# Performance work log

Hardware: AMD Instinct MI355X
Metric: run time of the kernel (lower is better)

The kernel has to match this reference:

```python
import jax, jax.numpy as jnp
import numpy as np

DIM = 384
WIN = 7
HEADS = 12
N = WIN * WIN  # 49
NUM_WINDOWS = 64
B_W = 2048


def _relative_position_index():
    coords = np.stack(np.meshgrid(np.arange(WIN), np.arange(WIN), indexing='ij'))  # (2,W,W)
    cf = coords.reshape(2, -1)  # (2,N)
    rel = cf[:, :, None] - cf[:, None, :]  # (2,N,N)
    rel = rel.transpose(1, 2, 0)
    rel[:, :, 0] += WIN - 1
    rel[:, :, 1] += WIN - 1
    rel[:, :, 0] *= 2 * WIN - 1
    return jnp.asarray(rel.sum(-1), dtype=jnp.int32)  # (N,N)


def setup_inputs() -> dict:
    key = jax.random.key(0)
    ks = jax.random.split(key, 8)
    x = jax.random.normal(ks[0], (B_W, N, DIM), dtype=jnp.float32)
    m = jax.random.uniform(ks[1], (NUM_WINDOWS, N, N))
    mask = jnp.where(m < 0.1, -100.0, 0.0).astype(jnp.float32)
    sd = 0.02
    qkv_w = jax.random.normal(ks[2], (DIM, 3 * DIM), dtype=jnp.float32) * sd
    qkv_b = jnp.zeros((3 * DIM,), dtype=jnp.float32)
    proj_w = jax.random.normal(ks[3], (DIM, DIM), dtype=jnp.float32) * sd
    proj_b = jnp.zeros((DIM,), dtype=jnp.float32)
    bias_table = jax.random.normal(ks[4], ((2 * WIN - 1) ** 2, HEADS), dtype=jnp.float32) * sd
    rel_idx = _relative_position_index()
    return {"x": x, "mask": mask, "qkv_w": qkv_w, "qkv_b": qkv_b,
            "proj_w": proj_w, "proj_b": proj_b, "bias_table": bias_table,
            "rel_idx": rel_idx}


def reference(x, mask, qkv_w, qkv_b, proj_w, proj_b, bias_table, rel_idx):
    Bw, n, C = x.shape
    H = HEADS
    hd = C // H
    scale = hd ** -0.5
    qkv = (x @ qkv_w + qkv_b).reshape(Bw, n, 3, H, hd)
    qkv = jnp.transpose(qkv, (2, 0, 3, 1, 4))  # (3, Bw, H, N, hd)
    q, k, v = qkv[0], qkv[1], qkv[2]
    attn = jnp.einsum('bhnd,bhmd->bhnm', q * scale, k)  # (Bw,H,N,N)
    bias = bias_table[rel_idx.reshape(-1)].reshape(n, n, H)
    attn = attn + jnp.transpose(bias, (2, 0, 1))[None]
    nW = mask.shape[0]
    attn = attn.reshape(Bw // nW, nW, H, n, n) + mask[None, :, None]
    attn = attn.reshape(Bw, H, n, n)
    attn = jax.nn.softmax(attn, axis=-1)
    out = jnp.einsum('bhnm,bhmd->bhnd', attn, v)
    out = jnp.transpose(out, (0, 2, 1, 3)).reshape(Bw, n, C)
    return out @ proj_w + proj_b
```

## Files before the change

### kernel.cpp

```cpp
#include <hip/hip_runtime.h>


#define DIMC   384
#define NTOK   49
#define NHEAD  12
#define HD     32
#define NWIN   64
#define BWIN   2048
#define SCALE  0.17677669529663687f

#define SLOT     4704
#define NBQ      9
#define NBP      3
#define FRAG_BLK 8192

#define WS_SLOTS ((size_t)BWIN * NHEAD * SLOT)
#define WS_BFRAG ((size_t)NBQ * 12 * FRAG_BLK)
#define WS_PFRAG ((size_t)NBP * 12 * FRAG_BLK)
#define WS_COMB  ((size_t)NWIN * NHEAD * NTOK * 64)
#define WS_NEED  ((WS_SLOTS + WS_BFRAG + WS_PFRAG) * 2 + WS_COMB * 4)

typedef short bf16x8 __attribute__((ext_vector_type(8)));
typedef unsigned short u16x8 __attribute__((ext_vector_type(8)));
typedef unsigned u32x4 __attribute__((ext_vector_type(4)));
typedef float f32x4  __attribute__((ext_vector_type(4)));

__device__ __forceinline__ unsigned short f2bf(float f) {
    union { float f; unsigned u; } v; v.f = f;
    unsigned r = v.u + 0x7fffu + ((v.u >> 16) & 1u);
    return (unsigned short)(r >> 16);
}
__device__ __forceinline__ float bf2f(unsigned short h) {
    union { unsigned u; float f; } v; v.u = ((unsigned)h) << 16;
    return v.f;
}
__device__ __forceinline__ void split2(float x, unsigned short& hi, unsigned short& lo) {
    hi = f2bf(x);
    lo = f2bf(x - bf2f(hi));
}
__device__ __forceinline__ unsigned cvtpk(float a, float b) {
    unsigned r;
    asm("v_cvt_pk_bf16_f32 %0, %1, %2" : "=v"(r) : "v"(a), "v"(b));
    return r;
}
__device__ __forceinline__ unsigned lopk(float a, float b, unsigned h) {
    union { unsigned u; float f; } h0, h1;
    h0.u = h << 16; h1.u = h & 0xffff0000u;
    return cvtpk(a - h0.f, b - h1.f);
}
__device__ __forceinline__ void splitpk8(float4 a, float4 b, u32x4& h, u32x4& l) {
    h[0] = cvtpk(a.x, a.y); h[1] = cvtpk(a.z, a.w);
    h[2] = cvtpk(b.x, b.y); h[3] = cvtpk(b.z, b.w);
    l[0] = lopk(a.x, a.y, h[0]); l[1] = lopk(a.z, a.w, h[1]);
    l[2] = lopk(b.x, b.y, h[2]); l[3] = lopk(b.z, b.w, h[3]);
}
__device__ __forceinline__ float4 ld4(const float* p) {
    return *reinterpret_cast<const float4*>(p);
}
__device__ __forceinline__ void gload16(const unsigned short* g, unsigned short* l) {
    __builtin_amdgcn_global_load_lds(
        (const __attribute__((address_space(1))) void*)g,
        (__attribute__((address_space(3))) void*)l, 16, 0, 0);
}

__global__ __launch_bounds__(256) void k_prep_w(
    const float* __restrict__ w, unsigned short* __restrict__ dst, int ncols)
{
    int f = blockIdx.x * 256 + threadIdx.x;
    if (f >= ncols * 48) return;
    int nb = f / 6144, rem = f - nb * 6144;
    int kc = rem >> 9, rem2 = rem & 511;
    int kq = rem2 >> 7, rl = rem2 & 127;
    int n = nb * 128 + rl, k0 = kc * 32 + kq * 8;
    u16x8 h8, l8;
    #pragma unroll
    for (int e = 0; e < 8; ++e) {
        unsigned short hh, ll;
        split2(w[(size_t)(k0 + e) * ncols + n], hh, ll);
        h8[e] = hh; l8[e] = ll;
    }
    size_t base = ((size_t)(nb * 12 + kc) << 13) + (size_t)((kq << 7) + rl) * 8;
    *reinterpret_cast<u16x8*>(&dst[base])        = h8;
    *reinterpret_cast<u16x8*>(&dst[base + 4096]) = l8;
}

__global__ __launch_bounds__(256) void k_prep_comb(
    const float* __restrict__ mask, const float* __restrict__ bias_table,
    const int* __restrict__ rel_idx, float* __restrict__ comb)
{
    int wh = blockIdx.x;
    int w = wh / NHEAD, h = wh - w * NHEAD;
    float* dst = comb + (size_t)wh * (NTOK * 64);
    for (int o = threadIdx.x; o < NTOK * 64; o += 256) {
        int i = o >> 6, j = o & 63;
        float v = -1e9f;
        if (j < NTOK) {
            int o2 = i * NTOK + j;
            v = mask[w * NTOK * NTOK + o2] + bias_table[rel_idx[o2] * NHEAD + h];
        }
        dst[o] = v;
    }
}

__global__ __launch_bounds__(256) void k_gemm_qkv(
    const float* __restrict__ x, const unsigned short* __restrict__ Bfrag,
    const float* __restrict__ qb, unsigned short* __restrict__ ws)
{
    __shared__ __align__(16) unsigned short Als[FRAG_BLK];
    __shared__ __align__(16) unsigned short Bls[FRAG_BLK];

    const int t = threadIdx.x;
    const int wave = t >> 6, l = t & 63, lj = l & 15, quad = l >> 4;
    const int wm = wave & 1, wn = wave >> 1;
    const int gm0 = blockIdx.y * 128, gn0 = blockIdx.x * 128;

    const int fs0 = t, fs1 = t + 256;
    const float* xp0 = x + (size_t)(gm0 + (fs0 & 127)) * DIMC + (fs0 >> 7) * 8;
    const float* xp1 = x + (size_t)(gm0 + (fs1 & 127)) * DIMC + (fs1 >> 7) * 8;
    const unsigned short* Bg = Bfrag + (size_t)blockIdx.x * 12 * FRAG_BLK;

    f32x4 acc[4][4];
    #pragma unroll
    for (int i = 0; i < 4; ++i)
        #pragma unroll
        for (int j = 0; j < 4; ++j) acc[i][j] = (f32x4)0.0f;

    for (int kc = 0; kc < 12; ++kc) {
        #pragma unroll
        for (int c = 0; c < 4; ++c) {
            int ch = wave * 4 + c;
            gload16(Bg + (size_t)kc * FRAG_BLK + ch * 512 + l * 8, &Bls[ch * 512]);
        }
        {
            float4 x0 = ld4(xp0 + kc * 32), x1 = ld4(xp0 + kc * 32 + 4);
            u32x4 h, lo;
            splitpk8(x0, x1, h, lo);
            *reinterpret_cast<u32x4*>(&Als[fs0 * 8])        = h;
            *reinterpret_cast<u32x4*>(&Als[4096 + fs0 * 8]) = lo;
        }
        {
            float4 x0 = ld4(xp1 + kc * 32), x1 = ld4(xp1 + kc * 32 + 4);
            u32x4 h, lo;
            splitpk8(x0, x1, h, lo);
            *reinterpret_cast<u32x4*>(&Als[fs1 * 8])        = h;
            *reinterpret_cast<u32x4*>(&Als[4096 + fs1 * 8]) = lo;
        }
        __syncthreads();

        bf16x8 ah[4], al[4], bh[4], bl[4];
        #pragma unroll
        for (int i = 0; i < 4; ++i) {
            int ra = (quad * 128 + wm * 64 + i * 16 + lj) * 8;
            ah[i] = *reinterpret_cast<const bf16x8*>(&Als[ra]);
            al[i] = *reinterpret_cast<const bf16x8*>(&Als[4096 + ra]);
            int rb = (quad * 128 + wn * 64 + i * 16 + lj) * 8;
            bh[i] = *reinterpret_cast<const bf16x8*>(&Bls[rb]);
            bl[i] = *reinterpret_cast<const bf16x8*>(&Bls[4096 + rb]);
        }
        #pragma unroll
        for (int tm = 0; tm < 4; ++tm)
            #pragma unroll
            for (int tn = 0; tn < 4; ++tn) {
                acc[tm][tn] = __builtin_amdgcn_mfma_f32_16x16x32_bf16(ah[tm], bh[tn], acc[tm][tn], 0, 0, 0);
                acc[tm][tn] = __builtin_amdgcn_mfma_f32_16x16x32_bf16(ah[tm], bl[tn], acc[tm][tn], 0, 0, 0);
                acc[tm][tn] = __builtin_amdgcn_mfma_f32_16x16x32_bf16(al[tm], bh[tn], acc[tm][tn], 0, 0, 0);
            }
        __syncthreads();
    }

    #pragma unroll
    for (int tn = 0; tn < 4; ++tn) {
        int col = gn0 + wn * 64 + tn * 16 + lj;
        float bias = qb[col];
        int part = col / 384, rem = col - part * 384;
        int h = rem >> 5, d = rem & 31;
        #pragma unroll
        for (int tm = 0; tm < 4; ++tm) {
            #pragma unroll
            for (int rr = 0; rr < 4; ++rr) {
                int row = gm0 + wm * 64 + tm * 16 + quad * 4 + rr;
                int b = row / 49, n = row - b * 49;
                size_t off = ((size_t)(b * NHEAD + h) * 3 + part) * 1568 + n * HD + d;
                ws[off] = f2bf(acc[tm][tn][rr] + bias);
            }
        }
    }
}

__global__ __launch_bounds__(128) void k_attn_mfma(
    unsigned short* __restrict__ ws, const float* __restrict__ comb)
{
    __shared__ __align__(16) unsigned short Pimg[2][8192];
    __shared__ __align__(16) unsigned short Vts[2][2048];

    const int t = threadIdx.x, wave = t >> 6, l = t & 63;
    const int lj = l & 15, quad = l >> 4;
    const int idx = blockIdx.x * 2 + wave;
    const int b = idx / NHEAD, h = idx - b * NHEAD;
    unsigned short* qp = ws + (size_t)idx * SLOT;
    const float* cb = comb + (size_t)((b & (NWIN - 1)) * NHEAD + h) * (NTOK * 64);
    unsigned short* pimg = Pimg[wave];
    unsigned short* vt   = Vts[wave];

    #pragma unroll
    for (int it = 0; it < 4; ++it)
        *reinterpret_cast<u16x8*>(&vt[it * 512 + l * 8]) = (u16x8)0;

    u16x8 vc[4];
    #pragma unroll
    for (int it = 0; it < 4; ++it) {
        int c = it * 64 + l;
        vc[it] = (c < 196)
            ? *reinterpret_cast<const u16x8*>(qp + 3136 + (c >> 2) * HD + (c & 3) * 8)
            : (u16x8)0;
    }

    bf16x8 aq[4], bk[4];
    #pragma unroll
    for (int mt = 0; mt < 4; ++mt) {
        int row = mt * 16 + lj;
        aq[mt] = (row < NTOK)
            ? *reinterpret_cast<const bf16x8*>(qp + row * HD + quad * 8) : (bf16x8)0;
        bk[mt] = (row < NTOK)
            ? *reinterpret_cast<const bf16x8*>(qp + 1568 + row * HD + quad * 8) : (bf16x8)0;
    }

    f32x4 s[4][4];
    #pragma unroll
    for (int mt = 0; mt < 4; ++mt)
        #pragma unroll
        for (int nt = 0; nt < 4; ++nt)
            s[mt][nt] = __builtin_amdgcn_mfma_f32_16x16x32_bf16(aq[mt], bk[nt], (f32x4)0.0f, 0, 0, 0);

    #pragma unroll
    for (int mt = 0; mt < 4; ++mt)
        #pragma unroll
        for (int r = 0; r < 4; ++r) {
            int i = mt * 16 + quad * 4 + r;
            #pragma unroll
            for (int nt = 0; nt < 4; ++nt) {
                float c = (i < NTOK) ? cb[i * 64 + nt * 16 + lj] : -1e9f;
                s[mt][nt][r] = fmaf(s[mt][nt][r], SCALE, c);
            }
        }

    __syncthreads();

    #pragma unroll
    for (int it = 0; it < 4; ++it) {
        int c = it * 64 + l;
        if (c < 196) {
            int j = c >> 2, dq = c & 3;
            #pragma unroll
            for (int e = 0; e < 8; ++e) {
                int d = dq * 8 + e;
                vt[(d * 64 + j) ^ ((d & 7) << 3)] = (unsigned short)vc[it][e];
            }
        }
    }

    #pragma unroll
    for (int mt = 0; mt < 4; ++mt)
        #pragma unroll
        for (int r = 0; r < 4; ++r) {
            float m = fmaxf(fmaxf(s[mt][0][r], s[mt][1][r]),
                            fmaxf(s[mt][2][r], s[mt][3][r]));
            m = fmaxf(m, __shfl_xor(m, 1));
            m = fmaxf(m, __shfl_xor(m, 2));
            m = fmaxf(m, __shfl_xor(m, 4));
            m = fmaxf(m, __shfl_xor(m, 8));
            float e0 = __expf(s[mt][0][r] - m), e1 = __expf(s[mt][1][r] - m);
            float e2 = __expf(s[mt][2][r] - m), e3 = __expf(s[mt][3][r] - m);
            float sum = (e0 + e1) + (e2 + e3);
            sum += __shfl_xor(sum, 1);
            sum += __shfl_xor(sum, 2);
            sum += __shfl_xor(sum, 4);
            sum += __shfl_xor(sum, 8);
            float inv = 1.0f / sum;
            int i = mt * 16 + quad * 4 + r;
            int swz = (i & 7) << 3;
            float p0 = e0 * inv, p1 = e1 * inv, p2 = e2 * inv, p3 = e3 * inv;
            unsigned short hh, ll;
            split2(p0, hh, ll);
            pimg[(i * 64 +  0 + lj) ^ swz] = hh; pimg[4096 + ((i * 64 +  0 + lj) ^ swz)] = ll;
            split2(p1, hh, ll);
            pimg[(i * 64 + 16 + lj) ^ swz] = hh; pimg[4096 + ((i * 64 + 16 + lj) ^ swz)] = ll;
            split2(p2, hh, ll);
            pimg[(i * 64 + 32 + lj) ^ swz] = hh; pimg[4096 + ((i * 64 + 32 + lj) ^ swz)] = ll;
            split2(p3, hh, ll);
            pimg[(i * 64 + 48 + lj) ^ swz] = hh; pimg[4096 + ((i * 64 + 48 + lj) ^ swz)] = ll;
        }

    __syncthreads();

    f32x4 o[4][2];
    #pragma unroll
    for (int mt = 0; mt < 4; ++mt) { o[mt][0] = (f32x4)0.0f; o[mt][1] = (f32x4)0.0f; }
    #pragma unroll
    for (int ks = 0; ks < 2; ++ks) {
        bf16x8 bv[2];
        #pragma unroll
        for (int nt = 0; nt < 2; ++nt) {
            int d = nt * 16 + lj;
            bv[nt] = *reinterpret_cast<const bf16x8*>(
                &vt[(d * 64 + ks * 32 + quad * 8) ^ ((d & 7) << 3)]);
        }
        #pragma unroll
        for (int mt = 0; mt < 4; ++mt) {
            int i = mt * 16 + lj;
            int fo = (i * 64 + ks * 32 + quad * 8) ^ ((i & 7) << 3);
            bf16x8 ph = *reinterpret_cast<const bf16x8*>(&pimg[fo]);
            bf16x8 pl = *reinterpret_cast<const bf16x8*>(&pimg[4096 + fo]);
            #pragma unroll
            for (int nt = 0; nt < 2; ++nt) {
                o[mt][nt] = __builtin_amdgcn_mfma_f32_16x16x32_bf16(ph, bv[nt], o[mt][nt], 0, 0, 0);
                o[mt][nt] = __builtin_amdgcn_mfma_f32_16x16x32_bf16(pl, bv[nt], o[mt][nt], 0, 0, 0);
            }
        }
    }

    #pragma unroll
    for (int mt = 0; mt < 4; ++mt)
        #pragma unroll
        for (int r = 0; r < 4; ++r) {
            int i = mt * 16 + quad * 4 + r;
            if (i < NTOK) {
                qp[i * HD + lj]      = f2bf(o[mt][0][r]);
                qp[i * HD + 16 + lj] = f2bf(o[mt][1][r]);
            }
        }
}

__global__ __launch_bounds__(256) void k_gemm_proj(
    const unsigned short* __restrict__ ws, const unsigned short* __restrict__ Pfrag,
    const float* __restrict__ pbias, float* __restrict__ out)
{
    __shared__ __align__(16) unsigned short Als[4096];
    __shared__ __align__(16) unsigned short Bls[FRAG_BLK];

    const int t = threadIdx.x;
    const int wave = t >> 6, l = t & 63, lj = l & 15, quad = l >> 4;
    const int wm = wave & 1, wn = wave >> 1;
    const int gm0 = blockIdx.y * 128, gn0 = blockIdx.x * 128;

    const int ch0 = wave * 2, ch1 = wave * 2 + 1;
    size_t abase0, abase1;
    {
        int fs = ch0 * 64 + l;
        int kq = fs >> 7, rl = fs & 127, row = gm0 + rl;
        int b = row / 49, n = row - b * 49;
        abase0 = (size_t)(b * NHEAD) * SLOT + n * HD + kq * 8;
    }
    {
        int fs = ch1 * 64 + l;
        int kq = fs >> 7, rl = fs & 127, row = gm0 + rl;
        int b = row / 49, n = row - b * 49;
        abase1 = (size_t)(b * NHEAD) * SLOT + n * HD + kq * 8;
    }
    const unsigned short* Bg = Pfrag + (size_t)blockIdx.x * 12 * FRAG_BLK;

    f32x4 acc[4][4];
    #pragma unroll
    for (int i = 0; i < 4; ++i)
        #pragma unroll
        for (int j = 0; j < 4; ++j) acc[i][j] = (f32x4)0.0f;

    for (int kc = 0; kc < 12; ++kc) {
        #pragma unroll
        for (int c = 0; c < 4; ++c) {
            int ch = wave * 4 + c;
            gload16(Bg + (size_t)kc * FRAG_BLK + ch * 512 + l * 8, &Bls[ch * 512]);
        }
        gload16(ws + abase0 + (size_t)kc * SLOT, &Als[ch0 * 512]);
        gload16(ws + abase1 + (size_t)kc * SLOT, &Als[ch1 * 512]);
        __syncthreads();

        bf16x8 a[4], bh[4], bl[4];
        #pragma unroll
        for (int i = 0; i < 4; ++i) {
            a[i] = *reinterpret_cast<const bf16x8*>(&Als[(quad * 128 + wm * 64 + i * 16 + lj) * 8]);
            int rb = (quad * 128 + wn * 64 + i * 16 + lj) * 8;
            bh[i] = *reinterpret_cast<const bf16x8*>(&Bls[rb]);
            bl[i] = *reinterpret_cast<const bf16x8*>(&Bls[4096 + rb]);
        }
        #pragma unroll
        for (int tm = 0; tm < 4; ++tm)
            #pragma unroll
            for (int tn = 0; tn < 4; ++tn) {
                acc[tm][tn] = __builtin_amdgcn_mfma_f32_16x16x32_bf16(a[tm], bh[tn], acc[tm][tn], 0, 0, 0);
                acc[tm][tn] = __builtin_amdgcn_mfma_f32_16x16x32_bf16(a[tm], bl[tn], acc[tm][tn], 0, 0, 0);
            }
        __syncthreads();
    }

    #pragma unroll
    for (int tn = 0; tn < 4; ++tn) {
        int col = gn0 + wn * 64 + tn * 16 + lj;
        float bias = pbias[col];
        #pragma unroll
        for (int tm = 0; tm < 4; ++tm)
            #pragma unroll
            for (int rr = 0; rr < 4; ++rr) {
                int row = gm0 + wm * 64 + tm * 16 + quad * 4 + rr;
                out[(size_t)row * DIMC + col] = acc[tm][tn][rr] + bias;
            }
    }
}

__global__ __launch_bounds__(192) void k_qkv_attn(
    const float* __restrict__ x, const float* __restrict__ mask,
    const float* __restrict__ qkv_w, const float* __restrict__ qkv_b,
    const float* __restrict__ bias_table, const int* __restrict__ rel_idx,
    float* __restrict__ out)
{
    __shared__ __align__(16) float xs_t[64 * 68];
    __shared__ __align__(16) float qs[NTOK * HD];
    __shared__ __align__(16) float ks_[NTOK * HD];
    __shared__ __align__(16) float vs[NTOK * HD];
    __shared__ __align__(16) union { float w[64 * 96]; float s[NTOK * 56]; } u;

    const int t = threadIdx.x, b = blockIdx.x;
    const int tx = t % 12, ty = t / 12;
    const float* xb = x + (size_t)b * NTOK * DIMC;
    const int mbase = (b % NWIN) * NTOK * NTOK;

    for (int h = 0; h < NHEAD; ++h) {
        float acc[4][8];
        #pragma unroll
        for (int r = 0; r < 4; ++r)
            #pragma unroll
            for (int cc = 0; cc < 8; ++cc) acc[r][cc] = 0.0f;
        for (int c0 = 0; c0 < DIMC; c0 += 64) {
            for (int idx = t; idx < NTOK * 64; idx += 192) {
                int i = idx >> 6, kk2 = idx & 63;
                xs_t[kk2 * 68 + i] = xb[i * DIMC + c0 + kk2];
            }
            for (int idx = t; idx < 64 * 96; idx += 192) {
                int kk2 = idx / 96, c = idx % 96;
                int col = (c >> 5) * DIMC + h * HD + (c & 31);
                u.w[kk2 * 96 + c] = qkv_w[(size_t)(c0 + kk2) * (3 * DIMC) + col];
            }
            __syncthreads();
            #pragma unroll 8
            for (int kk2 = 0; kk2 < 64; ++kk2) {
                const float4 xv = ld4(&xs_t[kk2 * 68 + ty * 4]);
                const float4 w0 = ld4(&u.w[kk2 * 96 + tx * 8]);
                const float4 w1 = ld4(&u.w[kk2 * 96 + tx * 8 + 4]);
                const float xr[4] = {xv.x, xv.y, xv.z, xv.w};
                const float wc[8] = {w0.x, w0.y, w0.z, w0.w, w1.x, w1.y, w1.z, w1.w};
                #pragma unroll
                for (int r = 0; r < 4; ++r)
                    #pragma unroll
                    for (int cc = 0; cc < 8; ++cc)
                        acc[r][cc] = fmaf(xr[r], wc[cc], acc[r][cc]);
            }
            __syncthreads();
        }
        {
            const int part = tx >> 2, cbase = (tx & 3) * 8;
            float* dst = (part == 0) ? qs : (part == 1) ? ks_ : vs;
            #pragma unroll
            for (int r = 0; r < 4; ++r) {
                int i = ty * 4 + r;
                if (i < NTOK)
                    #pragma unroll
                    for (int cc = 0; cc < 8; ++cc) {
                        int c5 = cbase + cc;
                        dst[i * HD + c5] = acc[r][cc] + qkv_b[part * DIMC + h * HD + c5];
                    }
            }
        }
        __syncthreads();
        for (int o = t; o < NTOK * NTOK; o += 192) {
            int i = o / 49, j = o % 49;
            float4 a4 = {0.f, 0.f, 0.f, 0.f};
            #pragma unroll
            for (int seg = 0; seg < 8; ++seg) {
                float4 q4 = ld4(&qs[i * HD + seg * 4]);
                float4 k4 = ld4(&ks_[j * HD + seg * 4]);
                a4.x = fmaf(q4.x, k4.x, a4.x); a4.y = fmaf(q4.y, k4.y, a4.y);
                a4.z = fmaf(q4.z, k4.z, a4.z); a4.w = fmaf(q4.w, k4.w, a4.w);
            }
            u.s[i * 56 + j] = (a4.x + a4.y + a4.z + a4.w) * SCALE
                            + bias_table[rel_idx[o] * NHEAD + h] + mask[mbase + o];
        }
        __syncthreads();
        if (t < NTOK) {
            float* row = &u.s[t * 56];
            float m = row[0];
            for (int j = 1; j < NTOK; ++j) m = fmaxf(m, row[j]);
            float ssum = 0.f;
            for (int j = 0; j < NTOK; ++j) { float e = __expf(row[j] - m); row[j] = e; ssum += e; }
            float inv = 1.0f / ssum;
            for (int j = 0; j < NTOK; ++j) row[j] *= inv;
        }
        __syncthreads();
        for (int o = t; o < NTOK * 8; o += 192) {
            int i = o >> 3, dg = o & 7;
            float4 a = {0.f, 0.f, 0.f, 0.f};
            for (int j = 0; j < NTOK; ++j) {
                float sj = u.s[i * 56 + j];
                float4 v4 = ld4(&vs[j * HD + dg * 4]);
                a.x = fmaf(sj, v4.x, a.x); a.y = fmaf(sj, v4.y, a.y);
                a.z = fmaf(sj, v4.z, a.z); a.w = fmaf(sj, v4.w, a.w);
            }
            *reinterpret_cast<float4*>(&out[(size_t)(b * NTOK + i) * DIMC + h * HD + dg * 4]) = a;
        }
        __syncthreads();
    }
}

__global__ __launch_bounds__(192) void k_proj(
    float* __restrict__ io, const float* __restrict__ proj_w,
    const float* __restrict__ proj_b)
{
    __shared__ __align__(16) float ys_t[DIMC * 20];
    __shared__ __align__(16) float wch[16 * DIMC];
    const int t = threadIdx.x, row0 = blockIdx.x * 16;
    const int tx = t % 48, ty = t / 48;
    for (int idx = t; idx < 16 * DIMC; idx += 192) {
        int i = idx / DIMC, k = idx % DIMC;
        ys_t[k * 20 + i] = io[(size_t)(row0 + i) * DIMC + k];
    }
    float acc[4][8];
    #pragma unroll
    for (int r = 0; r < 4; ++r)
        #pragma unroll
        for (int cc = 0; cc < 8; ++cc) acc[r][cc] = 0.0f;
    for (int k0 = 0; k0 < DIMC; k0 += 16) {
        for (int idx = t; idx < 16 * DIMC; idx += 192) {
            int kk2 = idx / DIMC, c = idx % DIMC;
            wch[kk2 * DIMC + c] = proj_w[(size_t)(k0 + kk2) * DIMC + c];
        }
        __syncthreads();
        #pragma unroll
        for (int kk2 = 0; kk2 < 16; ++kk2) {
            const float4 xv = ld4(&ys_t[(k0 + kk2) * 20 + ty * 4]);
            const float4 w0 = ld4(&wch[kk2 * DIMC + tx * 8]);
            const float4 w1 = ld4(&wch[kk2 * DIMC + tx * 8 + 4]);
            const float xr[4] = {xv.x, xv.y, xv.z, xv.w};
            const float wc[8] = {w0.x, w0.y, w0.z, w0.w, w1.x, w1.y, w1.z, w1.w};
            #pragma unroll
            for (int r = 0; r < 4; ++r)
                #pragma unroll
                for (int cc = 0; cc < 8; ++cc)
                    acc[r][cc] = fmaf(xr[r], wc[cc], acc[r][cc]);
        }
        __syncthreads();
    }
    #pragma unroll
    for (int r = 0; r < 4; ++r) {
        int i = ty * 4 + r;
        float* dst = &io[(size_t)(row0 + i) * DIMC + tx * 8];
        #pragma unroll
        for (int cc = 0; cc < 8; ++cc) dst[cc] = acc[r][cc] + proj_b[tx * 8 + cc];
    }
}

extern "C" void kernel_launch(void* const* d_in, const int* in_sizes, int n_in,
                              void* d_out, int out_size, void* d_ws, size_t ws_size,
                              hipStream_t stream) {
    const float* x          = (const float*)d_in[0];
    const float* mask       = (const float*)d_in[1];
    const float* qkv_w      = (const float*)d_in[2];
    const float* qkv_b      = (const float*)d_in[3];
    const float* proj_w     = (const float*)d_in[4];
    const float* proj_b     = (const float*)d_in[5];
    const float* bias_table = (const float*)d_in[6];
    const int*   rel_idx    = (const int*)d_in[7];
    float* out = (float*)d_out;

    if (ws_size >= WS_NEED) {
        unsigned short* ws = (unsigned short*)d_ws;
        unsigned short* Bf = ws + WS_SLOTS;
        unsigned short* Pf = Bf + WS_BFRAG;
        float* combf = (float*)(Pf + WS_PFRAG);
        k_prep_w<<<216, 256, 0, stream>>>(qkv_w, Bf, 3 * DIMC);
        k_prep_w<<<72, 256, 0, stream>>>(proj_w, Pf, DIMC);
        k_prep_comb<<<NWIN * NHEAD, 256, 0, stream>>>(mask, bias_table, rel_idx, combf);
        dim3 g1(9, 784);
        k_gemm_qkv<<<g1, 256, 0, stream>>>(x, Bf, qkv_b, ws);
        k_attn_mfma<<<(BWIN * NHEAD) / 2, 128, 0, stream>>>(ws, combf);
        dim3 g3(3, 784);
        k_gemm_proj<<<g3, 256, 0, stream>>>(ws, Pf, proj_b, out);
    } else {
        k_qkv_attn<<<BWIN, 192, 0, stream>>>(x, mask, qkv_w, qkv_b,
                                             bias_table, rel_idx, out);
        k_proj<<<(BWIN * NTOK) / 16, 192, 0, stream>>>(out, proj_w, proj_b);
    }
}
```

Before: 815.5 us.

## Pre-split x into bf16 hi/lo fragment layout and swizzle GEMM block order

```diff
diff --git a/kernel.cpp b/kernel.cpp
--- a/kernel.cpp
+++ b/kernel.cpp
@@ -12,13 +12,16 @@
 #define SLOT     4704
 #define NBQ      9
 #define NBP      3
+#define NRP      784
 #define FRAG_BLK 8192
 
 #define WS_SLOTS ((size_t)BWIN * NHEAD * SLOT)
 #define WS_BFRAG ((size_t)NBQ * 12 * FRAG_BLK)
 #define WS_PFRAG ((size_t)NBP * 12 * FRAG_BLK)
+#define WS_XFRAG ((size_t)NRP * 12 * FRAG_BLK)
 #define WS_COMB  ((size_t)NWIN * NHEAD * NTOK * 64)
-#define WS_NEED  ((WS_SLOTS + WS_BFRAG + WS_PFRAG) * 2 + WS_COMB * 4)
+#define WS_NEED_MID  ((WS_SLOTS + WS_BFRAG + WS_PFRAG) * 2 + WS_COMB * 4)
+#define WS_NEED_FULL (WS_NEED_MID + WS_XFRAG * 2)
 
 typedef short bf16x8 __attribute__((ext_vector_type(8)));
 typedef unsigned short u16x8 __attribute__((ext_vector_type(8)));
@@ -82,6 +85,36 @@
     size_t base = ((size_t)(nb * 12 + kc) << 13) + (size_t)((kq << 7) + rl) * 8;
     *reinterpret_cast<u16x8*>(&dst[base])        = h8;
     *reinterpret_cast<u16x8*>(&dst[base + 4096]) = l8;
+}
+
+__global__ __launch_bounds__(256) void k_prep_x(
+    const float* __restrict__ x, unsigned short* __restrict__ xf)
+{
+    __shared__ __align__(16) unsigned short H[4096], L[4096];
+    const int bid = blockIdx.x, rp = bid / 12, kc = bid - rp * 12;
+    const int t = threadIdx.x;
+    const int row0 = t >> 3, c4 = t & 7;
+    #pragma unroll
+    for (int p = 0; p < 4; ++p) {
+        int row = p * 32 + row0;
+        float4 v = ld4(x + (size_t)(rp * 128 + row) * DIMC + kc * 32 + c4 * 4);
+        unsigned h0 = cvtpk(v.x, v.y), h1 = cvtpk(v.z, v.w);
+        unsigned l0 = lopk(v.x, v.y, h0), l1 = lopk(v.z, v.w, h1);
+        int off = ((c4 >> 1) * 128 + row) * 8 + (c4 & 1) * 4;
+        *reinterpret_cast<unsigned*>(&H[off])     = h0;
+        *reinterpret_cast<unsigned*>(&H[off + 2]) = h1;
+        *reinterpret_cast<unsigned*>(&L[off])     = l0;
+        *reinterpret_cast<unsigned*>(&L[off + 2]) = l1;
+    }
+    __syncthreads();
+    unsigned short* dst = xf + (size_t)bid * FRAG_BLK;
+    #pragma unroll
+    for (int p = 0; p < 4; ++p) {
+        int o = p * 2048 + t * 8;
+        u16x8 v = (p < 2) ? *reinterpret_cast<const u16x8*>(&H[o])
+                          : *reinterpret_cast<const u16x8*>(&L[o - 4096]);
+        *reinterpret_cast<u16x8*>(&dst[p * 2048 + t * 8]) = v;
+    }
 }
 
 __global__ __launch_bounds__(256) void k_prep_comb(
@@ -99,6 +132,80 @@
             v = mask[w * NTOK * NTOK + o2] + bias_table[rel_idx[o2] * NHEAD + h];
         }
         dst[o] = v;
+    }
+}
+
+__global__ __launch_bounds__(256) void k_gemm_qkv_f(
+    const unsigned short* __restrict__ Xfrag, const unsigned short* __restrict__ Bfrag,
+    const float* __restrict__ qb, unsigned short* __restrict__ ws)
+{
+    __shared__ __align__(16) unsigned short Als[FRAG_BLK];
+    __shared__ __align__(16) unsigned short Bls[FRAG_BLK];
+
+    const int t = threadIdx.x;
+    const int wave = t >> 6, l = t & 63, lj = l & 15, quad = l >> 4;
+    const int wm = wave & 1, wn = wave >> 1;
+
+    const int bid = blockIdx.x;
+    const int lid = (bid & 7) * 882 + (bid >> 3);
+    const int rp = lid / 9, nb = lid - rp * 9;
+    const int gm0 = rp * 128, gn0 = nb * 128;
+
+    const unsigned short* Ag = Xfrag + (size_t)rp * 12 * FRAG_BLK;
+    const unsigned short* Bg = Bfrag + (size_t)nb * 12 * FRAG_BLK;
+
+    f32x4 acc[4][4];
+    #pragma unroll
+    for (int i = 0; i < 4; ++i)
+        #pragma unroll
+        for (int j = 0; j < 4; ++j) acc[i][j] = (f32x4)0.0f;
+
+    for (int kc = 0; kc < 12; ++kc) {
+        #pragma unroll
+        for (int c = 0; c < 4; ++c) {
+            int ch = wave * 4 + c;
+            gload16(Ag + (size_t)kc * FRAG_BLK + ch * 512 + l * 8, &Als[ch * 512]);
+            gload16(Bg + (size_t)kc * FRAG_BLK + ch * 512 + l * 8, &Bls[ch * 512]);
+        }
+        __syncthreads();
+
+        bf16x8 ah[4], al[4], bh[4], bl[4];
+        #pragma unroll
+        for (int i = 0; i < 4; ++i) {
+            int ra = (quad * 128 + wm * 64 + i * 16 + lj) * 8;
+            ah[i] = *reinterpret_cast<const bf16x8*>(&Als[ra]);
+            al[i] = *reinterpret_cast<const bf16x8*>(&Als[4096 + ra]);
+            int rb = (quad * 128 + wn * 64 + i * 16 + lj) * 8;
+            bh[i] = *reinterpret_cast<const bf16x8*>(&Bls[rb]);
+            bl[i] = *reinterpret_cast<const bf16x8*>(&Bls[4096 + rb]);
+        }
+        #pragma unroll
+        for (int tm = 0; tm < 4; ++tm)
+            #pragma unroll
+            for (int tn = 0; tn < 4; ++tn) {
+                acc[tm][tn] = __builtin_amdgcn_mfma_f32_16x16x32_bf16(ah[tm], bh[tn], acc[tm][tn], 0, 0, 0);
+                acc[tm][tn] = __builtin_amdgcn_mfma_f32_16x16x32_bf16(ah[tm], bl[tn], acc[tm][tn], 0, 0, 0);
+                acc[tm][tn] = __builtin_amdgcn_mfma_f32_16x16x32_bf16(al[tm], bh[tn], acc[tm][tn], 0, 0, 0);
+            }
+        __syncthreads();
+    }
+
+    #pragma unroll
+    for (int tn = 0; tn < 4; ++tn) {
+        int col = gn0 + wn * 64 + tn * 16 + lj;
+        float bias = qb[col];
+        int part = col / 384, rem = col - part * 384;
+        int h = rem >> 5, d = rem & 31;
+        #pragma unroll
+        for (int tm = 0; tm < 4; ++tm) {
+            #pragma unroll
+            for (int rr = 0; rr < 4; ++rr) {
+                int row = gm0 + wm * 64 + tm * 16 + quad * 4 + rr;
+                int b = row / 49, n = row - b * 49;
+                size_t off = ((size_t)(b * NHEAD + h) * 3 + part) * 1568 + n * HD + d;
+                ws[off] = f2bf(acc[tm][tn][rr] + bias);
+            }
+        }
     }
 }
 
@@ -341,7 +448,11 @@
     const int t = threadIdx.x;
     const int wave = t >> 6, l = t & 63, lj = l & 15, quad = l >> 4;
     const int wm = wave & 1, wn = wave >> 1;
-    const int gm0 = blockIdx.y * 128, gn0 = blockIdx.x * 128;
+
+    const int bid = blockIdx.x;
+    const int lid = (bid & 7) * 294 + (bid >> 3);
+    const int rp = lid / 3, nb = lid - rp * 3;
+    const int gm0 = rp * 128, gn0 = nb * 128;
 
     const int ch0 = wave * 2, ch1 = wave * 2 + 1;
     size_t abase0, abase1;
@@ -357,7 +468,7 @@
         int b = row / 49, n = row - b * 49;
         abase1 = (size_t)(b * NHEAD) * SLOT + n * HD + kq * 8;
     }
-    const unsigned short* Bg = Pfrag + (size_t)blockIdx.x * 12 * FRAG_BLK;
+    const unsigned short* Bg = Pfrag + (size_t)nb * 12 * FRAG_BLK;
 
     f32x4 acc[4][4];
     #pragma unroll
@@ -570,19 +681,24 @@
     const int*   rel_idx    = (const int*)d_in[7];
     float* out = (float*)d_out;
 
-    if (ws_size >= WS_NEED) {
+    if (ws_size >= WS_NEED_MID) {
         unsigned short* ws = (unsigned short*)d_ws;
         unsigned short* Bf = ws + WS_SLOTS;
         unsigned short* Pf = Bf + WS_BFRAG;
         float* combf = (float*)(Pf + WS_PFRAG);
+        unsigned short* Xf = (unsigned short*)(combf + WS_COMB);
         k_prep_w<<<216, 256, 0, stream>>>(qkv_w, Bf, 3 * DIMC);
         k_prep_w<<<72, 256, 0, stream>>>(proj_w, Pf, DIMC);
         k_prep_comb<<<NWIN * NHEAD, 256, 0, stream>>>(mask, bias_table, rel_idx, combf);
-        dim3 g1(9, 784);
-        k_gemm_qkv<<<g1, 256, 0, stream>>>(x, Bf, qkv_b, ws);
+        if (ws_size >= WS_NEED_FULL) {
+            k_prep_x<<<NRP * 12, 256, 0, stream>>>(x, Xf);
+            k_gemm_qkv_f<<<NRP * NBQ, 256, 0, stream>>>(Xf, Bf, qkv_b, ws);
+        } else {
+            dim3 g1(NBQ, NRP);
+            k_gemm_qkv<<<g1, 256, 0, stream>>>(x, Bf, qkv_b, ws);
+        }
         k_attn_mfma<<<(BWIN * NHEAD) / 2, 128, 0, stream>>>(ws, combf);
-        dim3 g3(3, 784);
-        k_gemm_proj<<<g3, 256, 0, stream>>>(ws, Pf, proj_b, out);
+        k_gemm_proj<<<NRP * NBP, 256, 0, stream>>>(ws, Pf, proj_b, out);
     } else {
         k_qkv_attn<<<BWIN, 192, 0, stream>>>(x, mask, qkv_w, qkv_b,
                                              bias_table, rel_idx, out);
```

After: 806.4 us. No clear change (-1.1%).
